# Kernel optimization log

Hardware: AMD Instinct MI355X
Metric: run time of the kernel (lower is better)

## Reference

```python
import jax, jax.numpy as jnp
import numpy as np

RADIUS = 3       # corr_radius
NUM_LEVELS = 4   # corr_lvls


def avg_pool2(x):
    """2x2 avg-pool with stride 2 on the last two axes (floor semantics, like F.avg_pool2d)."""
    nd = x.ndim
    s = jax.lax.reduce_window(
        x, 0.0, jax.lax.add,
        window_dimensions=(1,) * (nd - 2) + (2, 2),
        window_strides=(1,) * (nd - 2) + (2, 2),
        padding='VALID')
    return s * 0.25


def bilinear_window_lookup(corr, coords, radius):
    """corr: [B,H,W,hl,wl] per-pixel correlation maps; coords: [B,H,W,2] (x,y) in
    level-pixel units. Samples a (2r+1)^2 window around each coord with bilinear
    interpolation and zero padding (matches grid_sample align_corners=True, zeros).
    Returns [B,H,W,(2r+1)^2]."""
    B, H, W, hl, wl = corr.shape
    r = radius
    d = jnp.arange(-r, r + 1, dtype=coords.dtype)
    dy, dx = jnp.meshgrid(d, d, indexing='ij')
    delta = jnp.stack([dx.ravel(), dy.ravel()], axis=-1)        # [K2,2] (x,y)
    pts = coords[:, :, :, None, :] + delta                       # [B,H,W,K2,2]
    x, y = pts[..., 0], pts[..., 1]
    x0 = jnp.floor(x); y0 = jnp.floor(y)
    x1 = x0 + 1.0;     y1 = y0 + 1.0
    wx1 = x - x0; wx0 = 1.0 - wx1
    wy1 = y - y0; wy0 = 1.0 - wy1
    bi = jnp.arange(B)[:, None, None, None]
    hi = jnp.arange(H)[None, :, None, None]
    wi = jnp.arange(W)[None, None, :, None]

    def gather(xc, yc):
        valid = (xc >= 0) & (xc <= wl - 1) & (yc >= 0) & (yc <= hl - 1)
        xi = jnp.clip(xc, 0, wl - 1).astype(jnp.int32)
        yi = jnp.clip(yc, 0, hl - 1).astype(jnp.int32)
        return corr[bi, hi, wi, yi, xi] * valid.astype(corr.dtype)

    return (gather(x0, y0) * wx0 * wy0 + gather(x1, y0) * wx1 * wy0 +
            gather(x0, y1) * wx0 * wy1 + gather(x1, y1) * wx1 * wy1)


def pyramid_lookup(pyr, coords, radius):
    """pyr: list of [B,H,W,hl,wl]; coords: [B,H,W,2] at full level-0 resolution.
    Returns [B, L*(2r+1)^2, H, W]."""
    outs = [bilinear_window_lookup(c, coords / float(2 ** lvl), radius)
            for lvl, c in enumerate(pyr)]
    out = jnp.concatenate(outs, axis=-1)
    return jnp.transpose(out, (0, 3, 1, 2))


def setup_inputs() -> dict:
    key = jax.random.key(0)
    k0, k1, k2, k3, k4 = jax.random.split(key, 5)
    B, D, H, W = 1, 128, 60, 108  # 1/8-res features of a padded 480x864 frame
    fmap0 = jax.random.normal(k0, (B, D, H, W), dtype=jnp.float32)
    fmap1 = jax.random.normal(k1, (B, D, H, W), dtype=jnp.float32)
    flow0 = jax.random.normal(k2, (B, 2, H, W), dtype=jnp.float32)
    flow1 = jax.random.normal(k3, (B, 2, H, W), dtype=jnp.float32)
    embt = jax.random.uniform(k4, (B, 1, 1, 1), dtype=jnp.float32,
                              minval=0.1, maxval=0.9)
    return {"fmap0": fmap0, "fmap1": fmap1, "flow0": flow0,
            "flow1": flow1, "embt": embt}


def reference(fmap0, fmap1, flow0, flow1, embt):
    """BidirCorrBlock construction + AMT._corr_scale_lookup (downsample=1).
    Returns [B, 2*L*(2r+1)^2 + 4, H, W]: bidirectional multi-level correlation
    features concatenated with the stacked flows (corr, flow of the torch code)."""
    B, D, H, W = fmap0.shape
    # all-pairs correlation volume, scaled by 1/sqrt(D) as in RAFT's CorrBlock
    corr = jnp.einsum('bchw,bcuv->bhwuv', fmap0, fmap1) / jnp.sqrt(
        jnp.asarray(D, fmap0.dtype))                       # [B,H,W,H,W]
    corr_T = jnp.transpose(corr, (0, 3, 4, 1, 2))          # reversed direction
    pyr, pyr_T = [corr], [corr_T]
    for _ in range(NUM_LEVELS - 1):
        pyr.append(avg_pool2(pyr[-1]))
        pyr_T.append(avg_pool2(pyr_T[-1]))

    # coords_grid: channels (x, y)
    ys, xs = jnp.meshgrid(jnp.arange(H, dtype=fmap0.dtype),
                          jnp.arange(W, dtype=fmap0.dtype), indexing='ij')
    coord = jnp.broadcast_to(jnp.stack([xs, ys], axis=-1), (B, H, W, 2))

    t1_scale = 1.0 / embt           # [B,1,1,1]
    t0_scale = 1.0 / (1.0 - embt)
    f0 = jnp.transpose(flow0, (0, 2, 3, 1))  # [B,H,W,2]
    f1 = jnp.transpose(flow1, (0, 2, 3, 1))
    coords0 = coord + f1 * t1_scale          # lookup args of corr_fn(...)
    coords1 = coord + f0 * t0_scale

    corr0 = pyramid_lookup(pyr, coords0, RADIUS)     # [B, L*K2, H, W]
    corr1 = pyramid_lookup(pyr_T, coords1, RADIUS)
    corr_out = jnp.concatenate([corr0, corr1], axis=1)
    flow_out = jnp.concatenate([flow0, flow1], axis=1)
    return jnp.concatenate([corr_out, flow_out], axis=1)
```

## Files before the change

kernel.cpp:

```cpp
#include <hip/hip_runtime.h>

typedef _Float16 h16;
typedef __attribute__((ext_vector_type(2))) h16 h2v;
typedef __attribute__((ext_vector_type(8))) h16 h8v;

constexpr int H_ = 60, W_ = 108, HW_ = 6480;

constexpr unsigned B_F0T  = 0;
constexpr unsigned B_F1T  = 1658880;
constexpr unsigned B_F0L1 = 3317760;
constexpr unsigned B_F0L2 = 3732480;
constexpr unsigned B_F0L3 = 3836160;
constexpr unsigned B_F1L1 = 3859456;
constexpr unsigned B_F1L2 = 4274176;
constexpr unsigned B_F1L3 = 4377856;

__global__ __launch_bounds__(256) void k_transpose(const float* __restrict__ f0,
                                                   const float* __restrict__ f1,
                                                   h16* __restrict__ ws) {
    __shared__ float lds[64 * 129];
    const float* src = blockIdx.y ? f1 : f0;
    h16* dst = (h16*)((char*)ws + (blockIdx.y ? B_F1T : B_F0T));
    const int p0 = blockIdx.x * 64;
    const int t  = threadIdx.x;
    const int pr = t & 63, cr = t >> 6;
    #pragma unroll
    for (int cb = 0; cb < 128; cb += 4) {
        int c = cb + cr, p = p0 + pr;
        if (p < HW_) lds[pr * 129 + c] = src[(size_t)c * HW_ + p];
    }
    __syncthreads();
    const float S = 0.29730177875068026f;
    const int cw = t & 63, pw = t >> 6;
    #pragma unroll
    for (int pb = 0; pb < 64; pb += 4) {
        int p = p0 + pb + pw;
        if (p < HW_) {
            float a = lds[(pb + pw) * 129 + 2 * cw] * S;
            float b = lds[(pb + pw) * 129 + 2 * cw + 1] * S;
            h2v v; v.x = (h16)a; v.y = (h16)b;
            ((h2v*)dst)[(size_t)p * 64 + cw] = v;
        }
    }
}

__global__ __launch_bounds__(256) void k_pyramid(h16* __restrict__ wsh) {
    char* ws = (char*)wsh;
    const int map = blockIdx.y;
    const char* s = ws + (map ? B_F1T : B_F0T);
    const int bid = blockIdx.x;
    const int t = threadIdx.x;

    if (bid < 102) {
        const int idx = bid * 256 + t;
        if (idx >= 1620 * 16) return;
        const int pos = idx >> 4, q = idx & 15;
        const int y = pos / 54, x = pos - y * 54;
        const unsigned r0 = (unsigned)(2 * y * 108 + 2 * x) * 256 + q * 16;
        const unsigned r1 = r0 + 108 * 256;
        h8v a = *(const h8v*)(s + r0);
        h8v b = *(const h8v*)(s + r0 + 256);
        h8v c = *(const h8v*)(s + r1);
        h8v d = *(const h8v*)(s + r1 + 256);
        h8v o;
        #pragma unroll
        for (int k = 0; k < 8; ++k)
            o[k] = (h16)((((float)a[k] + (float)b[k]) + ((float)c[k] + (float)d[k])) * 0.25f);
        *(h8v*)(ws + (map ? B_F1L1 : B_F0L1) + (unsigned)pos * 256 + q * 16) = o;
    } else if (bid < 128) {
        const int idx = (bid - 102) * 256 + t;
        if (idx >= 405 * 16) return;
        const int pos = idx >> 4, q = idx & 15;
        const int y = pos / 27, x = pos - y * 27;
        float acc[8] = {};
        #pragma unroll
        for (int dy = 0; dy < 4; ++dy) {
            #pragma unroll
            for (int dx = 0; dx < 4; ++dx) {
                h8v u = *(const h8v*)(s + (unsigned)((4 * y + dy) * 108 + 4 * x + dx) * 256 + q * 16);
                #pragma unroll
                for (int k = 0; k < 8; ++k) acc[k] += (float)u[k];
            }
        }
        h8v o;
        #pragma unroll
        for (int k = 0; k < 8; ++k) o[k] = (h16)(acc[k] * 0.0625f);
        *(h8v*)(ws + (map ? B_F1L2 : B_F0L2) + (unsigned)pos * 256 + q * 16) = o;
    } else {
        const int idx = (bid - 128) * 256 + t;
        if (idx >= 91 * 128) return;
        const int pos = idx >> 7;
        const int sub = idx & 127;
        const int half = sub >> 6, lane = sub & 63;
        const int j = lane >> 3, qq = (lane & 7) + half * 8;
        const int y = pos / 13, x = pos - y * 13;
        float acc[8] = {};
        #pragma unroll
        for (int dx = 0; dx < 8; ++dx) {
            h8v u = *(const h8v*)(s + (unsigned)((8 * y + j) * 108 + 8 * x + dx) * 256 + qq * 16);
            #pragma unroll
            for (int k = 0; k < 8; ++k) acc[k] += (float)u[k];
        }
        #pragma unroll
        for (int k = 0; k < 8; ++k) {
            acc[k] += __shfl_xor(acc[k], 8);
            acc[k] += __shfl_xor(acc[k], 16);
            acc[k] += __shfl_xor(acc[k], 32);
        }
        if (j == 0) {
            h8v o;
            #pragma unroll
            for (int k = 0; k < 8; ++k) o[k] = (h16)(acc[k] * 0.015625f);
            *(h8v*)(ws + (map ? B_F1L3 : B_F0L3) + (unsigned)pos * 256 + qq * 16) = o;
        }
    }
}

template <int CTRL>
__device__ __forceinline__ float dpp_add(float x) {
    int y = __builtin_amdgcn_update_dpp(0, __builtin_bit_cast(int, x),
                                        CTRL, 0xF, 0xF, true);
    return x + __builtin_bit_cast(float, y);
}

__device__ __forceinline__ float dot_u4(uint4 u, uint4 s, float acc) {
    acc = __builtin_amdgcn_fdot2(__builtin_bit_cast(h2v, u.x),
                                 __builtin_bit_cast(h2v, s.x), acc, false);
    acc = __builtin_amdgcn_fdot2(__builtin_bit_cast(h2v, u.y),
                                 __builtin_bit_cast(h2v, s.y), acc, false);
    acc = __builtin_amdgcn_fdot2(__builtin_bit_cast(h2v, u.z),
                                 __builtin_bit_cast(h2v, s.z), acc, false);
    acc = __builtin_amdgcn_fdot2(__builtin_bit_cast(h2v, u.w),
                                 __builtin_bit_cast(h2v, s.w), acc, false);
    return acc;
}

__global__ __launch_bounds__(512, 2) void k_lookup2(const h16* __restrict__ wsh,
                                                    const float* __restrict__ flow0,
                                                    const float* __restrict__ flow1,
                                                    const float* __restrict__ embt,
                                                    float* __restrict__ out) {
    extern __shared__ char lds2[];
    const char* ws = (const char*)wsh;
    const int bid = blockIdx.x;
    const int xcd = bid & 7;
    const int dir = xcd >> 2;
    const int dirblk = (bid >> 3) * 4 + (xcd & 3);
    const int t = threadIdx.x;
    const int L = t & 63;
    const int wv = t >> 6;

    {
        const uint4* src = (const uint4*)(ws + (dir ? B_F0L2 : B_F1L2));
        #pragma unroll
        for (int i = 0; i < 16; ++i) {
            const int c = t + i * 512;
            if (c < 7936) ((uint4*)lds2)[c] = src[c];
        }
    }

    const float e = embt[0];
    const float scale = dir ? 1.0f / (1.0f - e) : 1.0f / e;
    const float* fl = dir ? flow0 : flow1;
    const unsigned sB  = dir ? B_F1T : B_F0T;
    const unsigned gB0 = dir ? B_F0T : B_F1T;
    const unsigned gB1 = dir ? B_F0L1 : B_F1L1;

    const int ch = L & 7;
    const int p  = L >> 3;

    __syncthreads();

    const int rbeg = (dirblk * 1620) >> 7;
    const int rend = ((dirblk + 1) * 1620) >> 7;

    for (int r = rbeg + wv; r < rend; r += 8) {
        const int px0 = r * 4;

        float cxa[4], cya[4];
        uint4 su0a[4], su1a[4];
        #pragma unroll
        for (int pp = 0; pp < 4; ++pp) {
            const int pix = px0 + pp;
            const int hh = pix / 108, ww = pix - hh * 108;
            cxa[pp] = (float)ww + fl[pix] * scale;
            cya[pp] = (float)hh + fl[HW_ + pix] * scale;
            const unsigned sbase = sB + (unsigned)pix * 256;
            su0a[pp] = *(const uint4*)(ws + sbase + ch * 16);
            su1a[pp] = *(const uint4*)(ws + sbase + 128 + ch * 16);
        }

        float vals[4][4];
        #pragma unroll
        for (int pp = 0; pp < 4; ++pp) {
            const float cx = cxa[pp], cy = cya[pp];
            const uint4 su0 = su0a[pp], su1 = su1a[pp];
            #pragma unroll
            for (int lvl = 0; lvl < 4; ++lvl) {
                const int wl = 108 >> lvl, hl = 60 >> lvl;
                const float inv = (lvl == 0) ? 1.f : (lvl == 1) ? 0.5f
                                : (lvl == 2) ? 0.25f : 0.125f;
                const float cxl = cx * inv, cyl = cy * inv;
                const float bxf = floorf(cxl), byf = floorf(cyl);
                const int bx = (int)bxf, by = (int)byf;
                const int gx = bx - 3 + p;
                const int gxc = min(max(gx, 0), wl - 1);
                const bool colv = (gx >= 0) & (gx < wl);
                const int gyo = by - 3 + ch;
                const bool ownv = colv & (gyo >= 0) & (gyo < hl);

                uint4 u0[8], u1[8];
                if (lvl >= 2) {
                    const char* base = (lvl == 3) ? (lds2 + 103680) : lds2;
                    const unsigned co = (unsigned)gxc * 256 + (unsigned)ch * 16;
                    #pragma unroll
                    for (int j = 0; j < 8; ++j) {
                        const int gy = by - 3 + j;
                        const int gyc = min(max(gy, 0), hl - 1);
                        const unsigned ro = co + (unsigned)(gyc * wl) * 256;
                        u0[j] = *(const uint4*)(base + ro);
                        u1[j] = *(const uint4*)(base + ro + 128);
                    }
                } else {
                    const unsigned gbase = (lvl == 0) ? gB0 : gB1;
                    const unsigned coloff = gbase + (unsigned)gxc * 256 + (unsigned)ch * 16;
                    #pragma unroll
                    for (int j = 0; j < 8; ++j) {
                        const int gy = by - 3 + j;
                        const int gyc = min(max(gy, 0), hl - 1);
                        const unsigned ro = coloff + (unsigned)(gyc * wl) * 256;
                        u0[j] = *(const uint4*)(ws + ro);
                        u1[j] = *(const uint4*)(ws + ro + 128);
                    }
                }

                float dval = 0.0f;
                #pragma unroll
                for (int j = 0; j < 8; ++j) {
                    float a0 = dot_u4(u0[j], su0, 0.0f);
                    float a1 = dot_u4(u1[j], su1, 0.0f);
                    float acc = a0 + a1;
                    acc = dpp_add<0xB1>(acc);
                    acc = dpp_add<0x4E>(acc);
                    acc = dpp_add<0x141>(acc);
                    dval = (ch == j) ? acc : dval;
                }
                dval = ownv ? dval : 0.0f;

                const int dyi = L / 7, dxi = L - dyi * 7;
                const float fx = cxl - bxf, fy = cyl - byf;
                const float d00 = __shfl(dval, 8 * dxi + dyi);
                const float d01 = __shfl(dval, 8 * dxi + dyi + 8);
                const float d10 = __shfl(dval, 8 * dxi + dyi + 1);
                const float d11 = __shfl(dval, 8 * dxi + dyi + 9);
                vals[lvl][pp] = (d00 * (1.0f - fx) + d01 * fx) * (1.0f - fy) +
                                (d10 * (1.0f - fx) + d11 * fx) * fy;
            }
        }

        #pragma unroll
        for (int lvl = 0; lvl < 4; ++lvl)
            if (L < 49)
                *(float4*)(out + (size_t)(dir * 196 + lvl * 49 + L) * HW_ + px0) =
                    make_float4(vals[lvl][0], vals[lvl][1], vals[lvl][2], vals[lvl][3]);
        if (dir == 0 && L >= 49 && L < 53) {
            const int c = L - 49;
            const float* f = (c < 2) ? flow0 + (size_t)c * HW_
                                     : flow1 + (size_t)(c - 2) * HW_;
            *(float4*)(out + (size_t)(392 + c) * HW_ + px0) = *(const float4*)(f + px0);
        }
    }
}

extern "C" void kernel_launch(void* const* d_in, const int* in_sizes, int n_in,
                              void* d_out, int out_size, void* d_ws, size_t ws_size,
                              hipStream_t stream) {
    const float* fmap0 = (const float*)d_in[0];
    const float* fmap1 = (const float*)d_in[1];
    const float* flow0 = (const float*)d_in[2];
    const float* flow1 = (const float*)d_in[3];
    const float* embt  = (const float*)d_in[4];
    h16* ws  = (h16*)d_ws;
    float* out = (float*)d_out;

    (void)hipFuncSetAttribute((const void*)k_lookup2,
                              hipFuncAttributeMaxDynamicSharedMemorySize, 126976);

    k_transpose<<<dim3(102, 2), 256, 0, stream>>>(fmap0, fmap1, ws);
    k_pyramid<<<dim3(174, 2), 256, 0, stream>>>(ws);
    k_lookup2<<<dim3(256), 512, 126976, stream>>>(ws, flow0, flow1, embt, out);
}
```

Before: 45.65 us.

## Use 1024-thread lookup blocks with one pixel per wave and LDS-staged output

The lookup kernel moves from 512-thread blocks that each handle four consecutive pixels per wave iteration to 1024-thread blocks in which 16 waves each handle up to four strided pixels, covering a contiguous pixel range per block. Results are staged through LDS, reusing the pyramid buffer after a barrier, and then written out coalesced per channel. The flow copy is done the same way. The aim is more parallelism per block and better-coalesced output stores. The cost is lower occupancy (one block per CU, a 1024-thread launch bound that limits registers), extra barriers, and scalar stores in place of float4 stores.

```diff
diff --git a/kernel.cpp b/kernel.cpp
--- a/kernel.cpp
+++ b/kernel.cpp
@@ -14,6 +14,9 @@
 constexpr unsigned B_F1L1 = 3859456;
 constexpr unsigned B_F1L2 = 4274176;
 constexpr unsigned B_F1L3 = 4377856;
+
+constexpr unsigned LDS_L3  = 103680;
+constexpr unsigned LDS_TOT = 126976;
 
 __global__ __launch_bounds__(256) void k_transpose(const float* __restrict__ f0,
                                                    const float* __restrict__ f1,
@@ -135,11 +138,11 @@
     return acc;
 }
 
-__global__ __launch_bounds__(512, 2) void k_lookup2(const h16* __restrict__ wsh,
-                                                    const float* __restrict__ flow0,
-                                                    const float* __restrict__ flow1,
-                                                    const float* __restrict__ embt,
-                                                    float* __restrict__ out) {
+__global__ __launch_bounds__(1024, 1) void k_lookup3(const h16* __restrict__ wsh,
+                                                     const float* __restrict__ flow0,
+                                                     const float* __restrict__ flow1,
+                                                     const float* __restrict__ embt,
+                                                     float* __restrict__ out) {
     extern __shared__ char lds2[];
     const char* ws = (const char*)wsh;
     const int bid = blockIdx.x;
@@ -153,11 +156,15 @@
     {
         const uint4* src = (const uint4*)(ws + (dir ? B_F0L2 : B_F1L2));
         #pragma unroll
-        for (int i = 0; i < 16; ++i) {
-            const int c = t + i * 512;
+        for (int i = 0; i < 8; ++i) {
+            const int c = t + i * 1024;
             if (c < 7936) ((uint4*)lds2)[c] = src[c];
         }
     }
+
+    const int rbeg = (dirblk * 6480) >> 7;
+    const int rend = ((dirblk + 1) * 6480) >> 7;
+    const int npix = rend - rbeg;
 
     const float e = embt[0];
     const float scale = dir ? 1.0f / (1.0f - e) : 1.0f / e;
@@ -171,30 +178,24 @@
 
     __syncthreads();
 
-    const int rbeg = (dirblk * 1620) >> 7;
-    const int rend = ((dirblk + 1) * 1620) >> 7;
-
-    for (int r = rbeg + wv; r < rend; r += 8) {
-        const int px0 = r * 4;
-
-        float cxa[4], cya[4];
-        uint4 su0a[4], su1a[4];
-        #pragma unroll
-        for (int pp = 0; pp < 4; ++pp) {
-            const int pix = px0 + pp;
+    float vals[4][4];
+
+    #pragma unroll
+    for (int ps = 0; ps < 4; ++ps) {
+        const int lpix = ps * 16 + wv;
+        const int pix = rbeg + lpix;
+        const bool act = (lpix < npix);
+
+        float cx = 0.f, cy = 0.f;
+        uint4 su0 = {}, su1 = {};
+        if (act) {
             const int hh = pix / 108, ww = pix - hh * 108;
-            cxa[pp] = (float)ww + fl[pix] * scale;
-            cya[pp] = (float)hh + fl[HW_ + pix] * scale;
+            cx = (float)ww + fl[pix] * scale;
+            cy = (float)hh + fl[HW_ + pix] * scale;
             const unsigned sbase = sB + (unsigned)pix * 256;
-            su0a[pp] = *(const uint4*)(ws + sbase + ch * 16);
-            su1a[pp] = *(const uint4*)(ws + sbase + 128 + ch * 16);
-        }
-
-        float vals[4][4];
-        #pragma unroll
-        for (int pp = 0; pp < 4; ++pp) {
-            const float cx = cxa[pp], cy = cya[pp];
-            const uint4 su0 = su0a[pp], su1 = su1a[pp];
+            su0 = *(const uint4*)(ws + sbase + ch * 16);
+            su1 = *(const uint4*)(ws + sbase + 128 + ch * 16);
+
             #pragma unroll
             for (int lvl = 0; lvl < 4; ++lvl) {
                 const int wl = 108 >> lvl, hl = 60 >> lvl;
@@ -206,12 +207,10 @@
                 const int gx = bx - 3 + p;
                 const int gxc = min(max(gx, 0), wl - 1);
                 const bool colv = (gx >= 0) & (gx < wl);
-                const int gyo = by - 3 + ch;
-                const bool ownv = colv & (gyo >= 0) & (gyo < hl);
 
                 uint4 u0[8], u1[8];
                 if (lvl >= 2) {
-                    const char* base = (lvl == 3) ? (lds2 + 103680) : lds2;
+                    const char* base = lds2 + ((lvl == 3) ? LDS_L3 : 0);
                     const unsigned co = (unsigned)gxc * 256 + (unsigned)ch * 16;
                     #pragma unroll
                     for (int j = 0; j < 8; ++j) {
@@ -222,7 +221,7 @@
                         u1[j] = *(const uint4*)(base + ro + 128);
                     }
                 } else {
-                    const unsigned gbase = (lvl == 0) ? gB0 : gB1;
+                    const unsigned gbase = lvl ? gB1 : gB0;
                     const unsigned coloff = gbase + (unsigned)gxc * 256 + (unsigned)ch * 16;
                     #pragma unroll
                     for (int j = 0; j < 8; ++j) {
@@ -237,15 +236,14 @@
                 float dval = 0.0f;
                 #pragma unroll
                 for (int j = 0; j < 8; ++j) {
-                    float a0 = dot_u4(u0[j], su0, 0.0f);
-                    float a1 = dot_u4(u1[j], su1, 0.0f);
-                    float acc = a0 + a1;
+                    float acc = dot_u4(u0[j], su0, 0.0f) + dot_u4(u1[j], su1, 0.0f);
                     acc = dpp_add<0xB1>(acc);
                     acc = dpp_add<0x4E>(acc);
                     acc = dpp_add<0x141>(acc);
                     dval = (ch == j) ? acc : dval;
                 }
-                dval = ownv ? dval : 0.0f;
+                const int gyo = by - 3 + ch;
+                dval = (colv & (gyo >= 0) & (gyo < hl)) ? dval : 0.0f;
 
                 const int dyi = L / 7, dxi = L - dyi * 7;
                 const float fx = cxl - bxf, fy = cyl - byf;
@@ -253,21 +251,41 @@
                 const float d01 = __shfl(dval, 8 * dxi + dyi + 8);
                 const float d10 = __shfl(dval, 8 * dxi + dyi + 1);
                 const float d11 = __shfl(dval, 8 * dxi + dyi + 9);
-                vals[lvl][pp] = (d00 * (1.0f - fx) + d01 * fx) * (1.0f - fy) +
+                vals[ps][lvl] = (d00 * (1.0f - fx) + d01 * fx) * (1.0f - fy) +
                                 (d10 * (1.0f - fx) + d11 * fx) * fy;
             }
         }
-
-        #pragma unroll
-        for (int lvl = 0; lvl < 4; ++lvl)
-            if (L < 49)
-                *(float4*)(out + (size_t)(dir * 196 + lvl * 49 + L) * HW_ + px0) =
-                    make_float4(vals[lvl][0], vals[lvl][1], vals[lvl][2], vals[lvl][3]);
-        if (dir == 0 && L >= 49 && L < 53) {
-            const int c = L - 49;
+    }
+
+    __syncthreads();
+
+    float* so = (float*)lds2;
+    if (L < 49) {
+        #pragma unroll
+        for (int ps = 0; ps < 4; ++ps) {
+            const int lpix = ps * 16 + wv;
+            if (lpix < npix) {
+                #pragma unroll
+                for (int lvl = 0; lvl < 4; ++lvl)
+                    so[(lvl * 49 + L) * 53 + lpix] = vals[ps][lvl];
+            }
+        }
+    }
+
+    __syncthreads();
+
+    for (int idx = t; idx < 196 * npix; idx += 1024) {
+        const int chn = idx / npix;
+        const int px  = idx - chn * npix;
+        out[(size_t)(dir * 196 + chn) * HW_ + rbeg + px] = so[chn * 53 + px];
+    }
+    if (dir == 0) {
+        for (int idx = t; idx < 4 * npix; idx += 1024) {
+            const int c  = idx / npix;
+            const int px = idx - c * npix;
             const float* f = (c < 2) ? flow0 + (size_t)c * HW_
                                      : flow1 + (size_t)(c - 2) * HW_;
-            *(float4*)(out + (size_t)(392 + c) * HW_ + px0) = *(const float4*)(f + px0);
+            out[(size_t)(392 + c) * HW_ + rbeg + px] = f[rbeg + px];
         }
     }
 }
@@ -283,10 +301,10 @@
     h16* ws  = (h16*)d_ws;
     float* out = (float*)d_out;
 
-    (void)hipFuncSetAttribute((const void*)k_lookup2,
-                              hipFuncAttributeMaxDynamicSharedMemorySize, 126976);
+    (void)hipFuncSetAttribute((const void*)k_lookup3,
+                              hipFuncAttributeMaxDynamicSharedMemorySize, LDS_TOT);
 
     k_transpose<<<dim3(102, 2), 256, 0, stream>>>(fmap0, fmap1, ws);
     k_pyramid<<<dim3(174, 2), 256, 0, stream>>>(ws);
-    k_lookup2<<<dim3(256), 512, 126976, stream>>>(ws, flow0, flow1, embt, out);
-}
+    k_lookup3<<<dim3(256), 1024, LDS_TOT, stream>>>(ws, flow0, flow1, embt, out);
+}
```

New measurement: 42.28 us. 7.4% less time.
